# Kernel optimization log

Hardware: AMD Instinct MI355X
Metric: run time of the kernel (lower is better)

## Reference

```python
import jax, jax.numpy as jnp
import numpy as np

HID = 3584      # hidden_size
NQ = 16         # num query heads
NKV = 8         # num kv heads
D = 256         # head_dim
SCALE = 256.0 ** -0.5   # query_pre_attn_scalar ** -0.5
CAP = 50.0      # attn_logits_soft_cap
WINDOW = 2048   # interleaved sliding window (even layer)
THETA = 10000.0
B, S = 1, 4096


def _rope(x, positions):
    """Neox-style RoPE. x: [B,S,N,D], positions: [B,S] int."""
    half = D // 2
    inv_freq = 1.0 / (THETA ** (jnp.arange(half, dtype=jnp.float32) / half))
    freqs = positions.astype(jnp.float32)[:, :, None] * inv_freq  # [B,S,half]
    cos = jnp.cos(freqs)[:, :, None, :]  # [B,S,1,half]
    sin = jnp.sin(freqs)[:, :, None, :]
    x1, x2 = x[..., :half], x[..., half:]
    return jnp.concatenate([x1 * cos - x2 * sin, x2 * cos + x1 * sin], axis=-1)


def setup_inputs() -> dict:
    key = jax.random.key(0)
    k1, k2, k3 = jax.random.split(key, 3)
    positions = jnp.broadcast_to(jnp.arange(S, dtype=jnp.int64)[None, :], (B, S))
    hidden_states = jax.random.normal(k1, (B, S, HID), dtype=jnp.float32)
    # scale weights ~ 1/sqrt(fan_in) so activations are O(1)
    w_qkv = jax.random.normal(k2, ((NQ + 2 * NKV) * D, HID), dtype=jnp.float32) * (HID ** -0.5)
    w_o = jax.random.normal(k3, (HID, NQ * D), dtype=jnp.float32) * ((NQ * D) ** -0.5)
    return {"positions": positions, "hidden_states": hidden_states, "w_qkv": w_qkv, "w_o": w_o}


def reference(positions, hidden_states, w_qkv, w_o):
    q_size, kv_size = NQ * D, NKV * D
    qkv = jnp.einsum('bsh,oh->bso', hidden_states, w_qkv)
    q = qkv[..., :q_size].reshape(B, S, NQ, D)
    k = qkv[..., q_size:q_size + kv_size].reshape(B, S, NKV, D)
    v = qkv[..., q_size + kv_size:].reshape(B, S, NKV, D)
    q = _rope(q, positions)
    k = _rope(k, positions)
    # GQA: repeat kv heads to match query heads
    g = NQ // NKV
    k = jnp.repeat(k, g, axis=2)  # [B,S,NQ,D]
    v = jnp.repeat(v, g, axis=2)
    scores = jnp.einsum('bqhd,bkhd->bhqk', q, k) * SCALE
    # Gemma2 logit soft-capping
    scores = CAP * jnp.tanh(scores / CAP)
    i = jnp.arange(S)[:, None]
    j = jnp.arange(S)[None, :]
    mask = (j <= i) & (i - j < WINDOW)  # causal + sliding window
    scores = jnp.where(mask, scores, -1e30)
    probs = jax.nn.softmax(scores, axis=-1)
    attn = jnp.einsum('bhqk,bkhd->bqhd', probs, v).reshape(B, S, NQ * D)
    return jnp.einsum('bso,ho->bsh', attn, w_o)
```

## Files before the change

kernel.cpp:

```cpp
#include <hip/hip_runtime.h>
#include <hip/hip_bf16.h>

typedef __bf16 bf16_t;
typedef __bf16 bf16x4 __attribute__((ext_vector_type(4)));
typedef __bf16 bf16x8 __attribute__((ext_vector_type(8)));
typedef float f32x4 __attribute__((ext_vector_type(4)));

#define HIDDEN 3584
#define NQH 16
#define NKVH 8
#define DH 256
#define SEQ 4096
#define QKV_COLS 8192
#define Q_SIZE 4096
#define KV_SIZE 2048
#define WINDOW 2048
#define SCALE_F 0.0625f
#define CAP_F 50.0f

__device__ __forceinline__ void gload16(const bf16_t* g, bf16_t* l) {
  __builtin_amdgcn_global_load_lds((__attribute__((address_space(1))) void*)g,
                                   (__attribute__((address_space(3))) void*)l, 16, 0, 0);
}

__global__ __launch_bounds__(256) void cvt_f32_to_bf16(const float* __restrict__ src,
                                                       bf16_t* __restrict__ dst, long n8) {
  long i = (long)blockIdx.x * 256 + threadIdx.x;
  if (i >= n8) return;
  const float4* s4 = (const float4*)src;
  float4 a = s4[i * 2];
  float4 b = s4[i * 2 + 1];
  bf16x8 o;
  o[0] = (bf16_t)a.x; o[1] = (bf16_t)a.y; o[2] = (bf16_t)a.z; o[3] = (bf16_t)a.w;
  o[4] = (bf16_t)b.x; o[5] = (bf16_t)b.y; o[6] = (bf16_t)b.z; o[7] = (bf16_t)b.w;
  *(bf16x8*)(dst + i * 8) = o;
}

#define TILE(T, WSTR, STAGE)                                                                \
  {                                                                                         \
    char* buf = lds + ((T) & 3) * 32768;                                                    \
    bf16x8 af[8], b0, b1, b2, b3;                                                           \
    _Pragma("unroll")                                                                       \
    for (int i = 0; i < 8; ++i) af[i] = *(const bf16x8*)(buf + aoff + i * 1024);            \
    b0 = *(const bf16x8*)(buf + boff);                                                      \
    b1 = *(const bf16x8*)(buf + boff + 1024);                                               \
    if (STAGE) {                                                                            \
      char* d = lds + (((T) + 3) & 3) * 32768;                                              \
      gload16(sA0 + ((T) + 3) * 32, (bf16_t*)(d + sdst0));                                  \
      gload16(sA1 + ((T) + 3) * 32, (bf16_t*)(d + 8192 + sdst0));                           \
    }                                                                                       \
    __builtin_amdgcn_s_setprio(1);                                                          \
    _Pragma("unroll")                                                                       \
    for (int i = 0; i < 8; ++i) {                                                           \
      acc[i][0] = __builtin_amdgcn_mfma_f32_16x16x32_bf16(af[i], b0, acc[i][0], 0, 0, 0);   \
      acc[i][1] = __builtin_amdgcn_mfma_f32_16x16x32_bf16(af[i], b1, acc[i][1], 0, 0, 0);   \
    }                                                                                       \
    __builtin_amdgcn_s_setprio(0);                                                          \
    __builtin_amdgcn_s_barrier();                                                           \
    b2 = *(const bf16x8*)(buf + boff + 2048);                                               \
    b3 = *(const bf16x8*)(buf + boff + 3072);                                               \
    if (STAGE) {                                                                            \
      char* d = lds + (((T) + 3) & 3) * 32768;                                              \
      gload16(sB0 + ((T) + 3) * 32, (bf16_t*)(d + 16384 + sdst0));                          \
      gload16(sB1 + ((T) + 3) * 32, (bf16_t*)(d + 24576 + sdst0));                          \
    }                                                                                       \
    __builtin_amdgcn_s_setprio(1);                                                          \
    _Pragma("unroll")                                                                       \
    for (int i = 0; i < 8; ++i) {                                                           \
      acc[i][2] = __builtin_amdgcn_mfma_f32_16x16x32_bf16(af[i], b2, acc[i][2], 0, 0, 0);   \
      acc[i][3] = __builtin_amdgcn_mfma_f32_16x16x32_bf16(af[i], b3, acc[i][3], 0, 0, 0);   \
    }                                                                                       \
    __builtin_amdgcn_s_setprio(0);                                                          \
    asm volatile("s_waitcnt vmcnt(" WSTR ")" ::: "memory");                                 \
    __builtin_amdgcn_s_barrier();                                                           \
  }

template <int K, bool OUT_BF16>
__global__ __launch_bounds__(512, 2) void gemm_bt(const bf16_t* __restrict__ A,
                                                  const bf16_t* __restrict__ B,
                                                  void* __restrict__ Cout, int N) {
  constexpr int NT = K / 32;
  __shared__ char lds[4 * 32768];
  int tid = threadIdx.x;
  int lane = tid & 63, w = tid >> 6;
  int wm = w >> 2, wn = w & 3;
  int r16 = lane & 15, g = lane >> 4;
  int bid = blockIdx.x;
  long bm = (long)((bid & 7) * 2 + ((bid >> 3) & 1)) * 256;
  long bn = (long)(bid >> 4) * 256;
  int ro = r16 >> 1;
  int asl = ((g + ((r16 & 1) << 2)) ^ ro) << 4;
  int aoff = wm * 8192 + ro * 128 + asl;
  int boff = 16384 + wn * 4096 + ro * 128 + asl;
  int slr = lane >> 3;
  int lc = (lane & 7) ^ slr;
  int kc8 = (lc & 3) * 8;
  long mr0 = (long)(w * 8 + slr) * 2 + (lc >> 2);
  long mr1 = mr0 + 128;
  const bf16_t* sA0 = A + (bm + mr0) * K + kc8;
  const bf16_t* sA1 = A + (bm + mr1) * K + kc8;
  const bf16_t* sB0 = B + (bn + mr0) * K + kc8;
  const bf16_t* sB1 = B + (bn + mr1) * K + kc8;
  int sdst0 = w * 1024;
  f32x4 acc[8][4] = {};
#pragma unroll
  for (int u = 0; u < 3; ++u) {
    char* d = lds + u * 32768;
    gload16(sA0 + u * 32, (bf16_t*)(d + sdst0));
    gload16(sA1 + u * 32, (bf16_t*)(d + 8192 + sdst0));
    gload16(sB0 + u * 32, (bf16_t*)(d + 16384 + sdst0));
    gload16(sB1 + u * 32, (bf16_t*)(d + 24576 + sdst0));
  }
  asm volatile("s_waitcnt vmcnt(8)" ::: "memory");
  __builtin_amdgcn_s_barrier();
  int t = 0;
  for (; t < NT - 3; ++t) TILE(t, "8", true);
  TILE(t, "4", false); ++t;
  TILE(t, "0", false); ++t;
  TILE(t, "0", false);
#pragma unroll
  for (int i = 0; i < 8; ++i)
#pragma unroll
    for (int j = 0; j < 4; ++j)
#pragma unroll
      for (int r = 0; r < 4; ++r) {
        long row = bm + wm * 128 + i * 16 + g * 4 + r;
        long col = bn + wn * 64 + j * 16 + r16;
        if (OUT_BF16) ((bf16_t*)Cout)[row * N + col] = (bf16_t)acc[i][j][r];
        else          ((float*)Cout)[row * N + col]  = acc[i][j][r];
      }
}

__global__ __launch_bounds__(256) void rope_kernel(bf16_t* __restrict__ qkv) {
  long idx = (long)blockIdx.x * 256 + threadIdx.x;
  int i = (int)(idx & 127);
  long rem = idx >> 7;
  int head = (int)(rem % 24);
  int s = (int)(rem / 24);
  int base = head < NQH ? head * DH : Q_SIZE + (head - NQH) * DH;
  long p1 = (long)s * QKV_COLS + base + i;
  long p2 = p1 + 128;
  float x1 = (float)qkv[p1], x2 = (float)qkv[p2];
  float inv_freq = exp2f((float)i * -0.10381025296522976f);
  float fr = (float)s * inv_freq;
  float sn, cs;
  sincosf(fr, &sn, &cs);
  qkv[p1] = (bf16_t)(x1 * cs - x2 * sn);
  qkv[p2] = (bf16_t)(x2 * cs + x1 * sn);
}

__global__ __launch_bounds__(256) void vtrans_kernel(const bf16_t* __restrict__ qkv,
                                                     bf16_t* __restrict__ vt) {
  __shared__ bf16_t tile[64][72];
  int t = threadIdx.x;
  long s0 = (long)blockIdx.x * 64;
  long c0 = (long)blockIdx.y * 64;
#pragma unroll
  for (int it = 0; it < 2; ++it) {
    int u = t + it * 256;
    int sr = u >> 3, ch = u & 7;
    bf16x8 v = *(const bf16x8*)&qkv[(s0 + sr) * QKV_COLS + (Q_SIZE + KV_SIZE) + c0 + ch * 8];
    *(bf16x8*)&tile[sr][ch * 8] = v;
  }
  __syncthreads();
#pragma unroll
  for (int it = 0; it < 2; ++it) {
    int u = t + it * 256;
    int cr = u >> 3, ch = u & 7;
    bf16x8 o;
#pragma unroll
    for (int j = 0; j < 8; ++j) o[j] = tile[ch * 8 + j][cr];
    *(bf16x8*)&vt[(c0 + cr) * SEQ + s0 + ch * 8] = o;
  }
}

__global__ __launch_bounds__(512, 2) void attn_kernel(const bf16_t* __restrict__ qkv,
                                                      const bf16_t* __restrict__ vt,
                                                      bf16_t* __restrict__ attn_out) {
  __shared__ bf16_t Kb[2][64 * 256];
  __shared__ bf16_t Vb[2][256 * 64];
  __shared__ bf16_t Pl[8 * 1024];
  int tid = threadIdx.x;
  int lane = tid & 63, w = tid >> 6;
  int r16 = lane & 15, g = lane >> 4;
  int bid = blockIdx.x;
  int swz = (bid & 7) * 64 + (bid >> 3);
  int h = swz >> 5;
  int qb = swz & 31;
  int kvh = h >> 1;
  int qw = qb * 128 + w * 16;
  bf16x8 qf[8];
  long qoff = (long)(qw + r16) * QKV_COLS + h * DH + g * 8;
#pragma unroll
  for (int kk = 0; kk < 8; ++kk) qf[kk] = *(const bf16x8*)&qkv[qoff + kk * 32];
  f32x4 acc[16] = {};
  float lsum[4] = {};
  const bf16_t* kg = qkv + Q_SIZE + (long)kvh * DH;
  const bf16_t* vg = vt + (long)kvh * DH * SEQ;
  bf16_t* pw = Pl + w * 1024;
  int lo = qb * 128 - (WINDOW - 1);
  int t0 = lo > 0 ? (lo >> 6) : 0;
  int t1 = qb * 2 + 2;
  int qlo = qw, qhi = qw + 15;

#define ATTN_STAGE(TT)                                                                   \
  {                                                                                      \
    int b_ = (TT) & 1;                                                                   \
    int kb_ = (TT) * 64;                                                                 \
    _Pragma("unroll")                                                                    \
    for (int c = 0; c < 4; ++c) {                                                        \
      int rowk = w * 8 + c * 2 + (lane >> 5);                                            \
      gload16(kg + (long)(kb_ + rowk) * QKV_COLS + (((lane & 31) ^ (rowk & 7)) * 8),     \
              &Kb[b_][w * 2048 + c * 512]);                                              \
      int rowv = w * 32 + c * 8 + (lane >> 3);                                           \
      gload16(vg + (long)rowv * SEQ + kb_ + (((lane & 7) ^ (rowv & 7)) * 8),             \
              &Vb[b_][w * 2048 + c * 512]);                                              \
    }                                                                                    \
  }

  ATTN_STAGE(t0);
  __syncthreads();
  for (int tt = t0; tt < t1; ++tt) {
    if (tt + 1 < t1) ATTN_STAGE(tt + 1);
    int b = tt & 1;
    int kb = tt * 64;
    bool active = !(kb > qhi || kb + 63 < qlo - (WINDOW - 1));
    if (active) {
      bool full = (kb + 63 <= qlo) && (qhi - kb <= WINDOW - 1);
      f32x4 sc[4] = {};
      __builtin_amdgcn_s_setprio(1);
#pragma unroll
      for (int kk = 0; kk < 8; ++kk) {
        int sl = ((kk * 4 + g) ^ (r16 & 7)) * 8;
#pragma unroll
        for (int c = 0; c < 4; ++c) {
          bf16x8 kf = *(const bf16x8*)&Kb[b][(c * 16 + r16) * 256 + sl];
          sc[c] = __builtin_amdgcn_mfma_f32_16x16x32_bf16(qf[kk], kf, sc[c], 0, 0, 0);
        }
      }
      __builtin_amdgcn_s_setprio(0);
#pragma unroll
      for (int c = 0; c < 4; ++c)
#pragma unroll
        for (int r = 0; r < 4; ++r) {
          float s = sc[c][r];
          float e = __expf(s * (2.0f * SCALE_F / CAP_F));
          float rr = __builtin_amdgcn_rcpf(e + 1.0f);
          float p = __expf(fmaf(-100.0f, rr, 38.0f));
          if (!full) {
            int q = qw + g * 4 + r;
            int k = kb + c * 16 + r16;
            p = ((k <= q) && (q - k < WINDOW)) ? p : 0.0f;
          }
          lsum[r] += p;
          int prow = g * 4 + r;
          int pbyte = prow * 128 + ((c * 32 + r16 * 2) ^ ((prow & 7) << 4));
          *(bf16_t*)((char*)pw + pbyte) = (bf16_t)p;
        }
      bf16x8 pa[2];
#pragma unroll
      for (int pk = 0; pk < 2; ++pk) {
        int pb = r16 * 128 + ((pk * 64 + g * 16) ^ ((r16 & 7) << 4));
        pa[pk] = *(const bf16x8*)((const char*)pw + pb);
      }
      __builtin_amdgcn_s_setprio(1);
#pragma unroll
      for (int dt = 0; dt < 16; ++dt) {
        int vrow = (dt * 16 + r16) * 64;
        bf16x8 vf0 = *(const bf16x8*)&Vb[b][vrow + ((g ^ (r16 & 7)) * 8)];
        acc[dt] = __builtin_amdgcn_mfma_f32_16x16x32_bf16(pa[0], vf0, acc[dt], 0, 0, 0);
        bf16x8 vf1 = *(const bf16x8*)&Vb[b][vrow + (((4 + g) ^ (r16 & 7)) * 8)];
        acc[dt] = __builtin_amdgcn_mfma_f32_16x16x32_bf16(pa[1], vf1, acc[dt], 0, 0, 0);
      }
      __builtin_amdgcn_s_setprio(0);
    }
    __syncthreads();
  }
  float inv[4];
#pragma unroll
  for (int r = 0; r < 4; ++r) {
    float s = lsum[r];
    s += __shfl_xor(s, 1);
    s += __shfl_xor(s, 2);
    s += __shfl_xor(s, 4);
    s += __shfl_xor(s, 8);
    inv[r] = 1.0f / s;
  }
#pragma unroll
  for (int dt = 0; dt < 16; ++dt)
#pragma unroll
    for (int r = 0; r < 4; ++r) {
      long row = qw + g * 4 + r;
      attn_out[row * Q_SIZE + h * DH + dt * 16 + r16] = (bf16_t)(acc[dt][r] * inv[r]);
    }
}

extern "C" void kernel_launch(void* const* d_in, const int* in_sizes, int n_in,
                              void* d_out, int out_size, void* d_ws, size_t ws_size,
                              hipStream_t stream) {
  const float* hid_f  = (const float*)d_in[1];
  const float* wqkv_f = (const float*)d_in[2];
  const float* wo_f   = (const float*)d_in[3];
  float* out = (float*)d_out;
  char* ws = (char*)d_ws;
  bf16_t* qkv    = (bf16_t*)(ws);
  bf16_t* wo_b   = (bf16_t*)(ws + 67108864);
  bf16_t* hid_b  = (bf16_t*)(ws + 96468992);
  bf16_t* wqkv_b = (bf16_t*)(ws + 125829120);
  bf16_t* attn_b = (bf16_t*)(ws + 96468992);
  bf16_t* vt     = (bf16_t*)(ws + 130023424);

  cvt_f32_to_bf16<<<7168, 256, 0, stream>>>(hid_f, hid_b, 14680064 / 8);
  cvt_f32_to_bf16<<<14336, 256, 0, stream>>>(wqkv_f, wqkv_b, 29360128 / 8);
  cvt_f32_to_bf16<<<7168, 256, 0, stream>>>(wo_f, wo_b, 14680064 / 8);
  gemm_bt<HIDDEN, true><<<512, 512, 0, stream>>>(hid_b, wqkv_b, qkv, QKV_COLS);
  rope_kernel<<<49152, 256, 0, stream>>>(qkv);
  vtrans_kernel<<<dim3(64, 32), 256, 0, stream>>>(qkv, vt);
  attn_kernel<<<512, 512, 0, stream>>>(qkv, vt, attn_b);
  gemm_bt<Q_SIZE, false><<<224, 512, 0, stream>>>(attn_b, wo_b, out, HIDDEN);
}
```

Baseline: 607.1 us.

## Swap MFMA operands for vectorized epilogue stores, vectorize RoPE, use exp2 in softmax

The MFMA A/B operands are swapped in both GEMM and attention so each lane holds four consecutive output columns. That allows 8- or 16-byte vector stores in the GEMM and attention epilogues, and the attention epilogue redistributes the per-row normalizer with a shuffle. The RoPE kernel now processes 8 elements per thread with bf16x8 loads and stores, using 8x fewer blocks. The soft-cap and softmax exponentials are rewritten with exp2f and pre-folded log2e constants. The main aim is to cut scattered 2-byte global stores, at the risk of subtle layout or indexing errors in the transposed fragments.

```diff
diff --git a/kernel.cpp b/kernel.cpp
--- a/kernel.cpp
+++ b/kernel.cpp
@@ -52,8 +52,8 @@
     __builtin_amdgcn_s_setprio(1);                                                          \
     _Pragma("unroll")                                                                       \
     for (int i = 0; i < 8; ++i) {                                                           \
-      acc[i][0] = __builtin_amdgcn_mfma_f32_16x16x32_bf16(af[i], b0, acc[i][0], 0, 0, 0);   \
-      acc[i][1] = __builtin_amdgcn_mfma_f32_16x16x32_bf16(af[i], b1, acc[i][1], 0, 0, 0);   \
+      acc[i][0] = __builtin_amdgcn_mfma_f32_16x16x32_bf16(b0, af[i], acc[i][0], 0, 0, 0);   \
+      acc[i][1] = __builtin_amdgcn_mfma_f32_16x16x32_bf16(b1, af[i], acc[i][1], 0, 0, 0);   \
     }                                                                                       \
     __builtin_amdgcn_s_setprio(0);                                                          \
     __builtin_amdgcn_s_barrier();                                                           \
@@ -67,8 +67,8 @@
     __builtin_amdgcn_s_setprio(1);                                                          \
     _Pragma("unroll")                                                                       \
     for (int i = 0; i < 8; ++i) {                                                           \
-      acc[i][2] = __builtin_amdgcn_mfma_f32_16x16x32_bf16(af[i], b2, acc[i][2], 0, 0, 0);   \
-      acc[i][3] = __builtin_amdgcn_mfma_f32_16x16x32_bf16(af[i], b3, acc[i][3], 0, 0, 0);   \
+      acc[i][2] = __builtin_amdgcn_mfma_f32_16x16x32_bf16(b2, af[i], acc[i][2], 0, 0, 0);   \
+      acc[i][3] = __builtin_amdgcn_mfma_f32_16x16x32_bf16(b3, af[i], acc[i][3], 0, 0, 0);   \
     }                                                                                       \
     __builtin_amdgcn_s_setprio(0);                                                          \
     asm volatile("s_waitcnt vmcnt(" WSTR ")" ::: "memory");                                 \
@@ -119,34 +119,46 @@
   TILE(t, "0", false); ++t;
   TILE(t, "0", false);
 #pragma unroll
-  for (int i = 0; i < 8; ++i)
-#pragma unroll
-    for (int j = 0; j < 4; ++j)
-#pragma unroll
-      for (int r = 0; r < 4; ++r) {
-        long row = bm + wm * 128 + i * 16 + g * 4 + r;
-        long col = bn + wn * 64 + j * 16 + r16;
-        if (OUT_BF16) ((bf16_t*)Cout)[row * N + col] = (bf16_t)acc[i][j][r];
-        else          ((float*)Cout)[row * N + col]  = acc[i][j][r];
+  for (int i = 0; i < 8; ++i) {
+    long row = bm + wm * 128 + i * 16 + r16;
+#pragma unroll
+    for (int j = 0; j < 4; ++j) {
+      long col = bn + wn * 64 + j * 16 + g * 4;
+      if (OUT_BF16) {
+        bf16x4 o;
+#pragma unroll
+        for (int r = 0; r < 4; ++r) o[r] = (bf16_t)acc[i][j][r];
+        *(bf16x4*)((bf16_t*)Cout + row * N + col) = o;
+      } else {
+        *(f32x4*)((float*)Cout + row * N + col) = acc[i][j];
       }
+    }
+  }
 }
 
 __global__ __launch_bounds__(256) void rope_kernel(bf16_t* __restrict__ qkv) {
   long idx = (long)blockIdx.x * 256 + threadIdx.x;
-  int i = (int)(idx & 127);
-  long rem = idx >> 7;
+  int i8 = (int)(idx & 15) * 8;
+  long rem = idx >> 4;
   int head = (int)(rem % 24);
   int s = (int)(rem / 24);
   int base = head < NQH ? head * DH : Q_SIZE + (head - NQH) * DH;
-  long p1 = (long)s * QKV_COLS + base + i;
-  long p2 = p1 + 128;
-  float x1 = (float)qkv[p1], x2 = (float)qkv[p2];
-  float inv_freq = exp2f((float)i * -0.10381025296522976f);
-  float fr = (float)s * inv_freq;
-  float sn, cs;
-  sincosf(fr, &sn, &cs);
-  qkv[p1] = (bf16_t)(x1 * cs - x2 * sn);
-  qkv[p2] = (bf16_t)(x2 * cs + x1 * sn);
+  long p1 = (long)s * QKV_COLS + base + i8;
+  bf16x8 x1 = *(const bf16x8*)&qkv[p1];
+  bf16x8 x2 = *(const bf16x8*)&qkv[p1 + 128];
+  bf16x8 o1, o2;
+#pragma unroll
+  for (int j = 0; j < 8; ++j) {
+    float inv_freq = exp2f((float)(i8 + j) * -0.10381025296522976f);
+    float fr = (float)s * inv_freq;
+    float sn, cs;
+    sincosf(fr, &sn, &cs);
+    float a = (float)x1[j], b = (float)x2[j];
+    o1[j] = (bf16_t)(a * cs - b * sn);
+    o2[j] = (bf16_t)(b * cs + a * sn);
+  }
+  *(bf16x8*)&qkv[p1] = o1;
+  *(bf16x8*)&qkv[p1 + 128] = o2;
 }
 
 __global__ __launch_bounds__(256) void vtrans_kernel(const bf16_t* __restrict__ qkv,
@@ -239,14 +251,17 @@
         }
       }
       __builtin_amdgcn_s_setprio(0);
+      const float C1 = 0.0036067376022224085f;
+      const float C2 = 144.26950408889634f;
+      const float C3 = 54.82241191667733f;
 #pragma unroll
       for (int c = 0; c < 4; ++c)
 #pragma unroll
         for (int r = 0; r < 4; ++r) {
           float s = sc[c][r];
-          float e = __expf(s * (2.0f * SCALE_F / CAP_F));
+          float e = exp2f(s * C1);
           float rr = __builtin_amdgcn_rcpf(e + 1.0f);
-          float p = __expf(fmaf(-100.0f, rr, 38.0f));
+          float p = exp2f(fmaf(-C2, rr, C3));
           if (!full) {
             int q = qw + g * 4 + r;
             int k = kb + c * 16 + r16;
@@ -268,9 +283,9 @@
       for (int dt = 0; dt < 16; ++dt) {
         int vrow = (dt * 16 + r16) * 64;
         bf16x8 vf0 = *(const bf16x8*)&Vb[b][vrow + ((g ^ (r16 & 7)) * 8)];
-        acc[dt] = __builtin_amdgcn_mfma_f32_16x16x32_bf16(pa[0], vf0, acc[dt], 0, 0, 0);
+        acc[dt] = __builtin_amdgcn_mfma_f32_16x16x32_bf16(vf0, pa[0], acc[dt], 0, 0, 0);
         bf16x8 vf1 = *(const bf16x8*)&Vb[b][vrow + (((4 + g) ^ (r16 & 7)) * 8)];
-        acc[dt] = __builtin_amdgcn_mfma_f32_16x16x32_bf16(pa[1], vf1, acc[dt], 0, 0, 0);
+        acc[dt] = __builtin_amdgcn_mfma_f32_16x16x32_bf16(vf1, pa[1], acc[dt], 0, 0, 0);
       }
       __builtin_amdgcn_s_setprio(0);
     }
@@ -286,13 +301,20 @@
     s += __shfl_xor(s, 8);
     inv[r] = 1.0f / s;
   }
-#pragma unroll
-  for (int dt = 0; dt < 16; ++dt)
-#pragma unroll
-    for (int r = 0; r < 4; ++r) {
-      long row = qw + g * 4 + r;
-      attn_out[row * Q_SIZE + h * DH + dt * 16 + r16] = (bf16_t)(acc[dt][r] * inv[r]);
-    }
+  int r3 = lane & 3;
+  float wv = inv[0];
+  wv = r3 == 1 ? inv[1] : wv;
+  wv = r3 == 2 ? inv[2] : wv;
+  wv = r3 == 3 ? inv[3] : wv;
+  float invq = __shfl(wv, ((lane & 15) >> 2) * 16 + (lane & 15));
+  long orow = (long)(qw + r16) * Q_SIZE + h * DH;
+#pragma unroll
+  for (int dt = 0; dt < 16; ++dt) {
+    bf16x4 o;
+#pragma unroll
+    for (int r = 0; r < 4; ++r) o[r] = (bf16_t)(acc[dt][r] * invq);
+    *(bf16x4*)&attn_out[orow + dt * 16 + g * 4] = o;
+  }
 }
 
 extern "C" void kernel_launch(void* const* d_in, const int* in_sizes, int n_in,
@@ -314,7 +336,7 @@
   cvt_f32_to_bf16<<<14336, 256, 0, stream>>>(wqkv_f, wqkv_b, 29360128 / 8);
   cvt_f32_to_bf16<<<7168, 256, 0, stream>>>(wo_f, wo_b, 14680064 / 8);
   gemm_bt<HIDDEN, true><<<512, 512, 0, stream>>>(hid_b, wqkv_b, qkv, QKV_COLS);
-  rope_kernel<<<49152, 256, 0, stream>>>(qkv);
+  rope_kernel<<<6144, 256, 0, stream>>>(qkv);
   vtrans_kernel<<<dim3(64, 32), 256, 0, stream>>>(qkv, vt);
   attn_kernel<<<512, 512, 0, stream>>>(qkv, vt, attn_b);
   gemm_bt<Q_SIZE, false><<<224, 512, 0, stream>>>(attn_b, wo_b, out, HIDDEN);
```

After: 639.7 us. 5.4% more time.
